# Kernel tuning notes

Hardware: AMD Instinct MI355X
Metric: run time of the kernel (lower is better)

The kernel has to match this reference:

```python
import jax, jax.numpy as jnp
import numpy as np
from jax import lax

B = 8192
HS = 64        # hidden_size (output channels)
HS4 = HS + 4   # internal channel count (68)
K = 3          # conv kernel size


def setup_inputs() -> dict:
    key = jax.random.key(0)
    ks = jax.random.split(key, 16)
    def n(k, shape, s=1.0):
        return jax.random.normal(k, shape, dtype=jnp.float32) * s
    return {
        "x": n(ks[0], (B, HS, 6, 6)),
        "cell": n(ks[1], (B, 2)),
        "interspace_coord": n(ks[2], (B, 2, 6, 6)),
        "conv1_w": n(ks[3], (HS4, HS4, K, K), 0.05),
        "conv1_b": n(ks[4], (HS4,), 0.05),
        "conv3_w": n(ks[5], (HS4, HS4, K, K), 0.05),
        "conv3_b": n(ks[6], (HS4,), 0.05),
        "lin5_w": n(ks[7], (9 * HS, HS4 * 25), 0.02),
        "lin5_b": n(ks[8], (9 * HS,), 0.02),
        "lin4_w": n(ks[9], (9 * HS, HS4 * 16), 0.02),
        "lin4_b": n(ks[10], (9 * HS,), 0.02),
        "lin3_w": n(ks[11], (9 * HS, HS4 * 9), 0.02),
        "lin3_b": n(ks[12], (9 * HS,), 0.02),
        "final_w": n(ks[13], (HS, 9 * HS), 0.02),
        "final_b": n(ks[14], (HS,), 0.02),
    }


def _conv(z, w, b):
    # torch Conv2d with padding=k//2, stride 1 == SAME conv, NCHW/OIHW
    y = lax.conv_general_dilated(z, w, (1, 1), 'SAME',
                                 dimension_numbers=('NCHW', 'OIHW', 'NCHW'))
    return y + b[None, :, None, None]


def _corners(z, ws):
    # four corner windows, stacked on a new leading axis (corner-major)
    H, W = z.shape[-2:]
    return jnp.stack([z[..., :ws, :ws],
                      z[..., :ws, W - ws:],
                      z[..., H - ws:, :ws],
                      z[..., H - ws:, W - ws:]], axis=0)


def reference(x, cell, interspace_coord,
              conv1_w, conv1_b, conv3_w, conv3_b,
              lin5_w, lin5_b, lin4_w, lin4_b, lin3_w, lin3_b,
              final_w, final_b):
    Bn = x.shape[0]
    new_cell = jnp.broadcast_to(cell.reshape(Bn, -1)[:, :, None, None],
                                (Bn, 2, 6, 6))
    lins = {5: (lin5_w, lin5_b), 4: (lin4_w, lin4_b), 3: (lin3_w, lin3_b)}
    for ws in (5, 4, 3):
        z = jnp.concatenate([x, new_cell, interspace_coord], axis=1)  # [B,68,6,6]
        z = _corners(z, ws).reshape(-1, HS4, ws, ws)                  # [4B,68,ws,ws]
        z = jnp.sin(z) + jnp.cos(z)
        z = jax.nn.relu(_conv(z, conv1_w, conv1_b))
        z = jnp.sin(z) + jnp.cos(z)
        z = jax.nn.relu(_conv(z, conv3_w, conv3_b)).reshape(4, Bn, -1)
        Wl, bl = lins[ws]
        z = jax.nn.relu(z @ Wl.T + bl).reshape(4, Bn, HS, 3, 3)
        m = jnp.concatenate([z[0], z[1]], axis=-1)   # [B,64,3,6]
        n = jnp.concatenate([z[2], z[3]], axis=-1)
        x = jnp.concatenate([m, n], axis=-2)          # [B,64,6,6]
    ew = 3
    c = _corners(x, ew)                               # [4,B,64,3,3]
    c = c.reshape(4 * Bn, -1) @ final_w.T + final_b   # [4B,64]
    c = c.reshape(Bn, HS, 2, 2)                       # same flat-order reshape as torch
    xc = x[:, :, ew - 1:ew + 1, ew - 1:ew + 1]        # center 2x2
    return (xc * c).reshape(Bn, HS, -1)
```

## Files before the change

kernel.cpp:

```cpp
#include <hip/hip_runtime.h>
#include <hip/hip_bf16.h>
#include <cstdint>
#include <cstddef>

#define BN 8192
#define MTOT 32768

using bf16 = __hip_bfloat16;
typedef float f32x4 __attribute__((ext_vector_type(4)));
typedef short short8 __attribute__((ext_vector_type(8)));

__device__ __forceinline__ bf16 f2b(float v) { return __float2bfloat16(v); }
__device__ __forceinline__ float b2f(bf16 v) { return __bfloat162float(v); }
__device__ __forceinline__ float sincos_sum(float x) {
    return 1.41421356237f * __sinf(x + 0.78539816340f);
}

template<int WS> struct WsCfg;
template<> struct WsCfg<5> { static constexpr int KD = 1728, NP = 1792, KTRUE = 1700; };
template<> struct WsCfg<4> { static constexpr int KD = 1088, NP = 1152, KTRUE = 1088; };
template<> struct WsCfg<3> { static constexpr int KD = 640,  NP = 640,  KTRUE = 612;  };

template<int WS, bool SRC_F32>
__global__ __launch_bounds__(256)
void zprep_block(const float* __restrict__ xF, const bf16* __restrict__ xB,
                 const float* __restrict__ cell, const float* __restrict__ isc,
                 bf16* __restrict__ Z, int m0g, int CM)
{
    constexpr int KD = WsCfg<WS>::KD;
    constexpr int KTRUE = 68 * WS * WS;
    const int b = blockIdx.x, tid = threadIdx.x;
    __shared__ float s[68][37];

    for (int i = tid; i < 64 * 36; i += 256) {
        int ic = i / 36, off = i % 36;
        size_t idx = ((size_t)b * 64 + ic) * 36 + off;
        float t = SRC_F32 ? xF[idx] : b2f(xB[idx]);
        s[ic][off] = sincos_sum(t);
    }
    if (tid < 2) {
        float t = sincos_sum(cell[b * 2 + tid]);
        #pragma unroll
        for (int off = 0; off < 36; off++) s[64 + tid][off] = t;
    }
    if (tid >= 64 && tid < 136) {
        int j = tid - 64;
        int ic = j / 36, off = j % 36;
        s[66 + ic][off] = sincos_sum(isc[((size_t)b * 2 + ic) * 36 + off]);
    }
    __syncthreads();

    for (int i = tid; i < 4 * KD; i += 256) {
        int q = i / KD, k = i % KD;
        int gm = q * BN + b;
        if (gm < m0g || gm >= m0g + CM) continue;
        float v = 0.f;
        if (k < KTRUE) {
            int pi = k / 68, ic = k % 68;
            int r = (q >> 1) * (6 - WS) + pi / WS;
            int c = (q & 1) * (6 - WS) + pi % WS;
            v = s[ic][r * 6 + c];
        }
        Z[(size_t)(gm - m0g) * KD + k] = f2b(v);
    }
}

template<int WS>
__global__ void build_wdense(const float* __restrict__ w1, const float* __restrict__ w3,
                             bf16* __restrict__ W1d, bf16* __restrict__ W3d)
{
    constexpr int KD = WsCfg<WS>::KD, NP = WsCfg<WS>::NP;
    constexpr int KTRUE = 68 * WS * WS;
    constexpr unsigned per = (unsigned)NP * (unsigned)KD;
    unsigned e = blockIdx.x * 256u + threadIdx.x;
    if (e >= 2u * per) return;
    const float* src = (e < per) ? w1 : w3;
    bf16* dst = (e < per) ? W1d : W3d;
    unsigned i = (e < per) ? e : (e - per);
    int n = (int)(i / (unsigned)KD), k = (int)(i % (unsigned)KD);
    float v = 0.f;
    if (n < KTRUE && k < KTRUE) {
        int po = n / 68, oc = n % 68, ro = po / WS, co = po % WS;
        int pi = k / 68, ic = k % 68, ri = pi / WS, ci = pi % WS;
        int kr = ri - ro + 1, kc = ci - co + 1;
        if (kr >= 0 && kr < 3 && kc >= 0 && kc < 3)
            v = src[((oc * 68 + ic) * 3 + kr) * 3 + kc];
    }
    dst[i] = f2b(v);
}

template<int WS>
__global__ void repack_lin(const float* __restrict__ wl, bf16* __restrict__ WlP)
{
    constexpr int KD = WsCfg<WS>::KD;
    constexpr int KTRUE = 68 * WS * WS;
    unsigned e = blockIdx.x * 256u + threadIdx.x;
    if (e >= 640u * (unsigned)KD) return;
    int n = (int)(e / (unsigned)KD), k = (int)(e % (unsigned)KD);
    float v = 0.f;
    if (n < 576 && k < KTRUE) {
        int pi = k / 68, ic = k % 68;
        v = wl[(size_t)n * KTRUE + ic * (WS * WS) + pi];
    }
    WlP[e] = f2b(v);
}

__global__ void repack_fin(const float* __restrict__ fw, bf16* __restrict__ WfP)
{
    unsigned e = blockIdx.x * 256u + threadIdx.x;
    if (e >= 128u * 576u) return;
    unsigned n = e / 576u, k = e % 576u;
    WfP[e] = (n < 64u) ? f2b(fw[n * 576u + k]) : f2b(0.f);
}

__global__ void build_bias(const float* __restrict__ b1, const float* __restrict__ b3,
                           const float* __restrict__ bl5, const float* __restrict__ bl4,
                           const float* __restrict__ bl3, const float* __restrict__ bfin,
                           float* __restrict__ bias)
{
    int e = blockIdx.x * 256 + threadIdx.x;
    if (e >= 9216) return;
    float v = 0.f;
    if (e < 1792)      { int n = e;        if (n < 1700) v = b1[n % 68]; }
    else if (e < 3584) { int n = e - 1792; if (n < 1700) v = b3[n % 68]; }
    else if (e < 4736) { int n = e - 3584; if (n < 1088) v = b1[n % 68]; }
    else if (e < 5888) { int n = e - 4736; if (n < 1088) v = b3[n % 68]; }
    else if (e < 6528) { int n = e - 5888; if (n < 612)  v = b1[n % 68]; }
    else if (e < 7168) { int n = e - 6528; if (n < 612)  v = b3[n % 68]; }
    else if (e < 7808) { int n = e - 7168; if (n < 576)  v = bl5[n]; }
    else if (e < 8448) { int n = e - 7808; if (n < 576)  v = bl4[n]; }
    else if (e < 9088) { int n = e - 8448; if (n < 576)  v = bl3[n]; }
    else               { int n = e - 9088; if (n < 64)   v = bfin[n]; }
    bias[e] = v;
}

__global__ void afin_prep(const bf16* __restrict__ xb, bf16* __restrict__ Afin,
                          int m_start, int CM)
{
    unsigned e = blockIdx.x * 256u + threadIdx.x;
    if (e >= (unsigned)CM * 576u) return;
    int lm = (int)(e / 576u), k = (int)(e % 576u);
    int m = m_start + lm;
    int q = m >> 13, b = m & (BN - 1);
    int ch = k / 9, p = k % 9, pr = p / 3, pc = p % 3;
    int r = (q >> 1) * 3 + pr, c = (q & 1) * 3 + pc;
    Afin[e] = xb[((size_t)b * 64 + ch) * 36 + r * 6 + c];
}

__device__ __forceinline__ void gload_lds16(const bf16* g, const bf16* lds_wave_base)
{
    unsigned off = (unsigned)(uintptr_t)lds_wave_base;
    off = __builtin_amdgcn_readfirstlane(off);
    __builtin_amdgcn_global_load_lds((const __attribute__((address_space(1))) unsigned int*)g,
                                     (__attribute__((address_space(3))) unsigned int*)off,
                                     16, 0, 0);
}

__device__ __forceinline__ int imin(int a, int b) { return a < b ? a : b; }
__device__ __forceinline__ int imax(int a, int b) { return a > b ? a : b; }

template<int EPI, int WS>
__global__ __launch_bounds__(256)
void gemm_bt(const bf16* __restrict__ A, const bf16* __restrict__ Bm, int KD,
             const float* __restrict__ bias,
             bf16* __restrict__ C, int ldc, int nlimit,
             int m0g, bf16* __restrict__ xbuf_out,
             const bf16* __restrict__ xbuf_xc, float* __restrict__ outp)
{
    __shared__ bf16 As[128 * 32];
    __shared__ bf16 Bs[128 * 32];
    const int tid = threadIdx.x;
    const int wave = tid >> 6, lane = tid & 63;
    const int l15 = lane & 15, lq = lane >> 4;
    const int wr = (wave >> 1) * 64, wc = (wave & 1) * 64;
    const int n0 = blockIdx.x * 128, m0 = blockIdx.y * 128;

    int klo = 0, khi = KD;
    if (WS > 0) {
        constexpr int ROWLEN = WS * 68;
        int po_lo = imin(n0 / 68, WS * WS - 1);
        int po_hi = imin((n0 + 127) / 68, WS * WS - 1);
        int r_lo = imax(po_lo / WS - 1, 0);
        int r_hi = imin(po_hi / WS + 1, WS - 1);
        klo = (r_lo * ROWLEN) & ~31;
        khi = imin(KD, ((r_hi + 1) * ROWLEN + 31) & ~31);
    }

    const bf16* Ab = A + (size_t)m0 * KD;
    const bf16* Bb = Bm + (size_t)n0 * KD;
    const int srow = tid >> 2, scol = (tid & 3) * 8;
    const bf16* aG0 = Ab + (size_t)srow * KD + scol;
    const bf16* aG1 = Ab + (size_t)(srow + 64) * KD + scol;
    const bf16* bG0 = Bb + (size_t)srow * KD + scol;
    const bf16* bG1 = Bb + (size_t)(srow + 64) * KD + scol;
    const bf16* lA0 = &As[wave * 512];
    const bf16* lA1 = &As[2048 + wave * 512];
    const bf16* lB0 = &Bs[wave * 512];
    const bf16* lB1 = &Bs[2048 + wave * 512];

    f32x4 acc[4][4];
    #pragma unroll
    for (int i = 0; i < 4; i++)
        #pragma unroll
        for (int j = 0; j < 4; j++) { f32x4 z = {0.f, 0.f, 0.f, 0.f}; acc[i][j] = z; }

    for (int k0 = klo; k0 < khi; k0 += 32) {
        gload_lds16(aG0 + k0, lA0);
        gload_lds16(aG1 + k0, lA1);
        gload_lds16(bG0 + k0, lB0);
        gload_lds16(bG1 + k0, lB1);
        __syncthreads();
        short8 af[4], bg[4];
        #pragma unroll
        for (int i = 0; i < 4; i++) af[i] = *(const short8*)&As[(wr + i * 16 + l15) * 32 + lq * 8];
        #pragma unroll
        for (int j = 0; j < 4; j++) bg[j] = *(const short8*)&Bs[(wc + j * 16 + l15) * 32 + lq * 8];
        #pragma unroll
        for (int i = 0; i < 4; i++)
            #pragma unroll
            for (int j = 0; j < 4; j++)
                acc[i][j] = __builtin_amdgcn_mfma_f32_16x16x32_bf16(af[i], bg[j], acc[i][j], 0, 0, 0);
        __syncthreads();
    }

    #pragma unroll
    for (int i = 0; i < 4; i++) {
        #pragma unroll
        for (int j = 0; j < 4; j++) {
            int n = n0 + wc + j * 16 + l15;
            #pragma unroll
            for (int r = 0; r < 4; r++) {
                int m = m0 + wr + i * 16 + lq * 4 + r;
                float v = acc[i][j][r];
                if (EPI == 0) {
                    if (n < nlimit) {
                        v += bias[n]; v = fmaxf(v, 0.f); v = sincos_sum(v);
                        C[(size_t)m * ldc + n] = f2b(v);
                    }
                } else if (EPI == 1) {
                    if (n < nlimit) {
                        v += bias[n]; v = fmaxf(v, 0.f);
                        C[(size_t)m * ldc + n] = f2b(v);
                    }
                } else if (EPI == 2) {
                    if (n < 576) {
                        v += bias[n]; v = fmaxf(v, 0.f);
                        int gm = m0g + m;
                        int q = gm >> 13, b = gm & (BN - 1);
                        int ch = n / 9, p = n % 9, rr = p / 3, cc = p % 3;
                        int R = rr + (q >> 1) * 3, Cc = cc + (q & 1) * 3;
                        xbuf_out[((size_t)b * 64 + ch) * 36 + R * 6 + Cc] = f2b(v);
                    }
                } else {
                    if (n < 64) {
                        v += bias[n];
                        int gm = m0g + m;
                        int f = gm * 64 + n;
                        int b2 = f >> 8, rem = f & 255;
                        int ch2 = rem >> 2, ii = (rem >> 1) & 1, jj = rem & 1;
                        float xc = b2f(xbuf_xc[((size_t)b2 * 64 + ch2) * 36 + (2 + ii) * 6 + (2 + jj)]);
                        outp[f] = v * xc;
                    }
                }
            }
        }
    }
}

template<int WS, bool SRC_F32>
static void run_ws(const float* xsrcF, const bf16* xsrcB, bf16* xdst,
                   const float* cell, const float* isc,
                   bf16* Za, bf16* Zb, const bf16* W1d, const bf16* W3d, const bf16* WlP,
                   const float* bias, int bo1, int bo3, int bol,
                   int nchunk, hipStream_t stream)
{
    constexpr int KD = WsCfg<WS>::KD, NP = WsCfg<WS>::NP;
    int CM = MTOT / nchunk;
    for (int c = 0; c < nchunk; c++) {
        int m0g = c * CM;
        zprep_block<WS, SRC_F32><<<BN, 256, 0, stream>>>(
            xsrcF, xsrcB, cell, isc, Za, m0g, CM);
        dim3 g12(NP / 128, CM / 128);
        gemm_bt<0, WS><<<g12, 256, 0, stream>>>(Za, W1d, KD, bias + bo1, Zb, KD, KD,
                                                0, nullptr, nullptr, nullptr);
        gemm_bt<1, WS><<<g12, 256, 0, stream>>>(Zb, W3d, KD, bias + bo3, Za, KD, KD,
                                                0, nullptr, nullptr, nullptr);
        dim3 g3(5, CM / 128);
        gemm_bt<2, 0><<<g3, 256, 0, stream>>>(Za, WlP, KD, bias + bol, nullptr, 0, 0,
                                              m0g, xdst, nullptr, nullptr);
    }
}

extern "C" void kernel_launch(void* const* d_in, const int* in_sizes, int n_in,
                              void* d_out, int out_size, void* d_ws, size_t ws_size,
                              hipStream_t stream)
{
    const float* x    = (const float*)d_in[0];
    const float* cell = (const float*)d_in[1];
    const float* isc  = (const float*)d_in[2];
    const float* c1w  = (const float*)d_in[3];
    const float* c1b  = (const float*)d_in[4];
    const float* c3w  = (const float*)d_in[5];
    const float* c3b  = (const float*)d_in[6];
    const float* l5w  = (const float*)d_in[7];
    const float* l5b  = (const float*)d_in[8];
    const float* l4w  = (const float*)d_in[9];
    const float* l4b  = (const float*)d_in[10];
    const float* l3w  = (const float*)d_in[11];
    const float* l3b  = (const float*)d_in[12];
    const float* fw   = (const float*)d_in[13];
    const float* fb   = (const float*)d_in[14];

    char* base = (char*)d_ws;
    size_t cur = 0;
    auto take = [&](size_t bytes) -> char* {
        char* r = base + cur; cur += (bytes + 255) & ~(size_t)255; return r;
    };

    const size_t XB = (size_t)BN * 64 * 36 * 2;
    size_t wbytes = 2 * (1792ull * 1728 + 1152ull * 1088 + 640ull * 640) * 2
                  + (640ull * 1728 + 640ull * 1088 + 640ull * 640) * 2
                  + 128ull * 576 * 2 + 9216ull * 4 + 64 * 256;
    auto need = [&](int nc) -> size_t {
        size_t xb = (nc > 1) ? 2 * XB : XB;
        return xb + wbytes + 2 * ((size_t)(MTOT / nc) * 1728 * 2);
    };
    int nchunk = (ws_size >= need(1)) ? 1 : (ws_size >= need(2)) ? 2
               : (ws_size >= need(4)) ? 4 : 8;

    bf16* xbufA = (bf16*)take(XB);
    bf16* xbufB = (nchunk > 1) ? (bf16*)take(XB) : xbufA;
    bf16* w1d5 = (bf16*)take(1792ull * 1728 * 2);
    bf16* w3d5 = (bf16*)take(1792ull * 1728 * 2);
    bf16* w1d4 = (bf16*)take(1152ull * 1088 * 2);
    bf16* w3d4 = (bf16*)take(1152ull * 1088 * 2);
    bf16* w1d3 = (bf16*)take(640ull * 640 * 2);
    bf16* w3d3 = (bf16*)take(640ull * 640 * 2);
    bf16* wl5p = (bf16*)take(640ull * 1728 * 2);
    bf16* wl4p = (bf16*)take(640ull * 1088 * 2);
    bf16* wl3p = (bf16*)take(640ull * 640 * 2);
    bf16* wfp  = (bf16*)take(128ull * 576 * 2);
    float* biasb = (float*)take(9216ull * 4);
    int CM = MTOT / nchunk;
    bf16* Za = (bf16*)take((size_t)CM * 1728 * 2);
    bf16* Zb = (bf16*)take((size_t)CM * 1728 * 2);
    bf16* Afin = Za;

    auto nb = [](size_t t) { return dim3((unsigned)((t + 255) / 256)); };
    build_wdense<5><<<nb(2ull * 1792 * 1728), 256, 0, stream>>>(c1w, c3w, w1d5, w3d5);
    build_wdense<4><<<nb(2ull * 1152 * 1088), 256, 0, stream>>>(c1w, c3w, w1d4, w3d4);
    build_wdense<3><<<nb(2ull * 640 * 640), 256, 0, stream>>>(c1w, c3w, w1d3, w3d3);
    repack_lin<5><<<nb(640ull * 1728), 256, 0, stream>>>(l5w, wl5p);
    repack_lin<4><<<nb(640ull * 1088), 256, 0, stream>>>(l4w, wl4p);
    repack_lin<3><<<nb(640ull * 640), 256, 0, stream>>>(l3w, wl3p);
    repack_fin<<<nb(128ull * 576), 256, 0, stream>>>(fw, wfp);
    build_bias<<<36, 256, 0, stream>>>(c1b, c3b, l5b, l4b, l3b, fb, biasb);

    run_ws<5, true >(x, nullptr, xbufA, cell, isc, Za, Zb, w1d5, w3d5, wl5p, biasb, 0,    1792, 7168, nchunk, stream);
    run_ws<4, false>(nullptr, xbufA, xbufB, cell, isc, Za, Zb, w1d4, w3d4, wl4p, biasb, 3584, 4736, 7808, nchunk, stream);
    run_ws<3, false>(nullptr, xbufB, xbufA, cell, isc, Za, Zb, w1d3, w3d3, wl3p, biasb, 5888, 6528, 8448, nchunk, stream);

    for (int c = 0; c < nchunk; c++) {
        int m0g = c * CM;
        afin_prep<<<nb((size_t)CM * 576), 256, 0, stream>>>(xbufA, Afin, m0g, CM);
        gemm_bt<3, 0><<<dim3(1, CM / 128), 256, 0, stream>>>(Afin, wfp, 576, biasb + 9088,
                                                             nullptr, 0, 0, m0g, nullptr,
                                                             xbufA, (float*)d_out);
    }
}
```

Baseline: 1.462 ms.

## Use XCD-aware atomic tile scheduling and a 64-wide K step in the GEMMs

```diff
diff --git a/kernel.cpp b/kernel.cpp
--- a/kernel.cpp
+++ b/kernel.cpp
@@ -159,21 +159,50 @@
 __device__ __forceinline__ int imin(int a, int b) { return a < b ? a : b; }
 __device__ __forceinline__ int imax(int a, int b) { return a > b ? a : b; }
 
+__device__ __forceinline__ int get_xcd()
+{
+    int x;
+    asm volatile("s_getreg_b32 %0, hwreg(HW_REG_XCC_ID)" : "=s"(x));
+    return x & 7;
+}
+
 template<int EPI, int WS>
 __global__ __launch_bounds__(256)
 void gemm_bt(const bf16* __restrict__ A, const bf16* __restrict__ Bm, int KD,
-             const float* __restrict__ bias,
+             const float* __restrict__ bias, int ntiles, int mt8, int quota,
+             unsigned* __restrict__ cnt,
              bf16* __restrict__ C, int ldc, int nlimit,
              int m0g, bf16* __restrict__ xbuf_out,
              const bf16* __restrict__ xbuf_xc, float* __restrict__ outp)
 {
-    __shared__ bf16 As[128 * 32];
-    __shared__ bf16 Bs[128 * 32];
+    __shared__ bf16 As[2 * 128 * 64];
+    __shared__ bf16 Bs[2 * 128 * 64];
+    __shared__ int s_tile;
     const int tid = threadIdx.x;
+
+    if (tid == 0) {
+        int xcd = get_xcd();
+        int t = -1;
+        for (int pass = 0; pass < 16 && t < 0; pass++) {
+            for (int k = 0; k < 8 && t < 0; k++) {
+                int q = (xcd + k) & 7;
+                unsigned idx = atomicAdd(&cnt[q], 1u);
+                if (idx < (unsigned)quota) t = q * quota + (int)idx;
+            }
+        }
+        if (t < 0) t = (int)blockIdx.x;
+        s_tile = t;
+    }
+    __syncthreads();
+    const int tile = s_tile;
+    const int qx = tile / quota, lt = tile % quota;
+    const int m_idx = qx * mt8 + lt / ntiles;
+    const int n_idx = lt % ntiles;
+    const int n0 = n_idx * 128, m0 = m_idx * 128;
+
     const int wave = tid >> 6, lane = tid & 63;
     const int l15 = lane & 15, lq = lane >> 4;
     const int wr = (wave >> 1) * 64, wc = (wave & 1) * 64;
-    const int n0 = blockIdx.x * 128, m0 = blockIdx.y * 128;
 
     int klo = 0, khi = KD;
     if (WS > 0) {
@@ -182,9 +211,13 @@
         int po_hi = imin((n0 + 127) / 68, WS * WS - 1);
         int r_lo = imax(po_lo / WS - 1, 0);
         int r_hi = imin(po_hi / WS + 1, WS - 1);
-        klo = (r_lo * ROWLEN) & ~31;
-        khi = imin(KD, ((r_hi + 1) * ROWLEN + 31) & ~31);
-    }
+        klo = (r_lo * ROWLEN) & ~63;
+        khi = imin(KD, ((r_hi + 1) * ROWLEN + 63) & ~63);
+    }
+
+    float bj[4];
+    #pragma unroll
+    for (int j = 0; j < 4; j++) bj[j] = bias[n0 + wc + j * 16 + l15];
 
     const bf16* Ab = A + (size_t)m0 * KD;
     const bf16* Bb = Bm + (size_t)n0 * KD;
@@ -193,10 +226,6 @@
     const bf16* aG1 = Ab + (size_t)(srow + 64) * KD + scol;
     const bf16* bG0 = Bb + (size_t)srow * KD + scol;
     const bf16* bG1 = Bb + (size_t)(srow + 64) * KD + scol;
-    const bf16* lA0 = &As[wave * 512];
-    const bf16* lA1 = &As[2048 + wave * 512];
-    const bf16* lB0 = &Bs[wave * 512];
-    const bf16* lB1 = &Bs[2048 + wave * 512];
 
     f32x4 acc[4][4];
     #pragma unroll
@@ -204,22 +233,30 @@
         #pragma unroll
         for (int j = 0; j < 4; j++) { f32x4 z = {0.f, 0.f, 0.f, 0.f}; acc[i][j] = z; }
 
-    for (int k0 = klo; k0 < khi; k0 += 32) {
-        gload_lds16(aG0 + k0, lA0);
-        gload_lds16(aG1 + k0, lA1);
-        gload_lds16(bG0 + k0, lB0);
-        gload_lds16(bG1 + k0, lB1);
+    for (int k0 = klo; k0 < khi; k0 += 64) {
+        #pragma unroll
+        for (int c = 0; c < 2; c++) {
+            gload_lds16(aG0 + k0 + c * 32, &As[c * 4096 + wave * 512]);
+            gload_lds16(aG1 + k0 + c * 32, &As[c * 4096 + 2048 + wave * 512]);
+            gload_lds16(bG0 + k0 + c * 32, &Bs[c * 4096 + wave * 512]);
+            gload_lds16(bG1 + k0 + c * 32, &Bs[c * 4096 + 2048 + wave * 512]);
+        }
         __syncthreads();
-        short8 af[4], bg[4];
         #pragma unroll
-        for (int i = 0; i < 4; i++) af[i] = *(const short8*)&As[(wr + i * 16 + l15) * 32 + lq * 8];
-        #pragma unroll
-        for (int j = 0; j < 4; j++) bg[j] = *(const short8*)&Bs[(wc + j * 16 + l15) * 32 + lq * 8];
-        #pragma unroll
-        for (int i = 0; i < 4; i++)
+        for (int c = 0; c < 2; c++) {
+            short8 af[4], bg[4];
+            #pragma unroll
+            for (int i = 0; i < 4; i++)
+                af[i] = *(const short8*)&As[c * 4096 + (wr + i * 16 + l15) * 32 + lq * 8];
             #pragma unroll
             for (int j = 0; j < 4; j++)
-                acc[i][j] = __builtin_amdgcn_mfma_f32_16x16x32_bf16(af[i], bg[j], acc[i][j], 0, 0, 0);
+                bg[j] = *(const short8*)&Bs[c * 4096 + (wc + j * 16 + l15) * 32 + lq * 8];
+            #pragma unroll
+            for (int i = 0; i < 4; i++)
+                #pragma unroll
+                for (int j = 0; j < 4; j++)
+                    acc[i][j] = __builtin_amdgcn_mfma_f32_16x16x32_bf16(af[i], bg[j], acc[i][j], 0, 0, 0);
+        }
         __syncthreads();
     }
 
@@ -234,17 +271,17 @@
                 float v = acc[i][j][r];
                 if (EPI == 0) {
                     if (n < nlimit) {
-                        v += bias[n]; v = fmaxf(v, 0.f); v = sincos_sum(v);
+                        v += bj[j]; v = fmaxf(v, 0.f); v = sincos_sum(v);
                         C[(size_t)m * ldc + n] = f2b(v);
                     }
                 } else if (EPI == 1) {
                     if (n < nlimit) {
-                        v += bias[n]; v = fmaxf(v, 0.f);
+                        v += bj[j]; v = fmaxf(v, 0.f);
                         C[(size_t)m * ldc + n] = f2b(v);
                     }
                 } else if (EPI == 2) {
                     if (n < 576) {
-                        v += bias[n]; v = fmaxf(v, 0.f);
+                        v += bj[j]; v = fmaxf(v, 0.f);
                         int gm = m0g + m;
                         int q = gm >> 13, b = gm & (BN - 1);
                         int ch = n / 9, p = n % 9, rr = p / 3, cc = p % 3;
@@ -253,7 +290,7 @@
                     }
                 } else {
                     if (n < 64) {
-                        v += bias[n];
+                        v += bj[j];
                         int gm = m0g + m;
                         int f = gm * 64 + n;
                         int b2 = f >> 8, rem = f & 255;
@@ -272,22 +309,22 @@
                    const float* cell, const float* isc,
                    bf16* Za, bf16* Zb, const bf16* W1d, const bf16* W3d, const bf16* WlP,
                    const float* bias, int bo1, int bo3, int bol,
-                   int nchunk, hipStream_t stream)
+                   int nchunk, unsigned* cnts, int* cset, hipStream_t stream)
 {
     constexpr int KD = WsCfg<WS>::KD, NP = WsCfg<WS>::NP;
     int CM = MTOT / nchunk;
+    int mt = CM / 128, mt8 = mt / 8;
     for (int c = 0; c < nchunk; c++) {
         int m0g = c * CM;
         zprep_block<WS, SRC_F32><<<BN, 256, 0, stream>>>(
             xsrcF, xsrcB, cell, isc, Za, m0g, CM);
-        dim3 g12(NP / 128, CM / 128);
-        gemm_bt<0, WS><<<g12, 256, 0, stream>>>(Za, W1d, KD, bias + bo1, Zb, KD, KD,
-                                                0, nullptr, nullptr, nullptr);
-        gemm_bt<1, WS><<<g12, 256, 0, stream>>>(Zb, W3d, KD, bias + bo3, Za, KD, KD,
-                                                0, nullptr, nullptr, nullptr);
-        dim3 g3(5, CM / 128);
-        gemm_bt<2, 0><<<g3, 256, 0, stream>>>(Za, WlP, KD, bias + bol, nullptr, 0, 0,
-                                              m0g, xdst, nullptr, nullptr);
+        int nt12 = NP / 128, q12 = nt12 * mt8;
+        gemm_bt<0, WS><<<nt12 * mt, 256, 0, stream>>>(Za, W1d, KD, bias + bo1,
+            nt12, mt8, q12, cnts + 8 * (*cset)++, Zb, KD, KD, 0, nullptr, nullptr, nullptr);
+        gemm_bt<1, WS><<<nt12 * mt, 256, 0, stream>>>(Zb, W3d, KD, bias + bo3,
+            nt12, mt8, q12, cnts + 8 * (*cset)++, Za, KD, KD, 0, nullptr, nullptr, nullptr);
+        gemm_bt<2, 0><<<5 * mt, 256, 0, stream>>>(Za, WlP, KD, bias + bol,
+            5, mt8, 5 * mt8, cnts + 8 * (*cset)++, nullptr, 0, 0, m0g, xdst, nullptr, nullptr);
     }
 }
 
@@ -320,7 +357,7 @@
     const size_t XB = (size_t)BN * 64 * 36 * 2;
     size_t wbytes = 2 * (1792ull * 1728 + 1152ull * 1088 + 640ull * 640) * 2
                   + (640ull * 1728 + 640ull * 1088 + 640ull * 640) * 2
-                  + 128ull * 576 * 2 + 9216ull * 4 + 64 * 256;
+                  + 128ull * 576 * 2 + 9216ull * 4 + 128ull * 8 * 4 + 64 * 256;
     auto need = [&](int nc) -> size_t {
         size_t xb = (nc > 1) ? 2 * XB : XB;
         return xb + wbytes + 2 * ((size_t)(MTOT / nc) * 1728 * 2);
@@ -341,10 +378,13 @@
     bf16* wl3p = (bf16*)take(640ull * 640 * 2);
     bf16* wfp  = (bf16*)take(128ull * 576 * 2);
     float* biasb = (float*)take(9216ull * 4);
+    unsigned* cnts = (unsigned*)take(128ull * 8 * 4);
     int CM = MTOT / nchunk;
     bf16* Za = (bf16*)take((size_t)CM * 1728 * 2);
     bf16* Zb = (bf16*)take((size_t)CM * 1728 * 2);
     bf16* Afin = Za;
+
+    hipMemsetAsync(cnts, 0, 128ull * 8 * 4, stream);
 
     auto nb = [](size_t t) { return dim3((unsigned)((t + 255) / 256)); };
     build_wdense<5><<<nb(2ull * 1792 * 1728), 256, 0, stream>>>(c1w, c3w, w1d5, w3d5);
@@ -356,15 +396,20 @@
     repack_fin<<<nb(128ull * 576), 256, 0, stream>>>(fw, wfp);
     build_bias<<<36, 256, 0, stream>>>(c1b, c3b, l5b, l4b, l3b, fb, biasb);
 
-    run_ws<5, true >(x, nullptr, xbufA, cell, isc, Za, Zb, w1d5, w3d5, wl5p, biasb, 0,    1792, 7168, nchunk, stream);
-    run_ws<4, false>(nullptr, xbufA, xbufB, cell, isc, Za, Zb, w1d4, w3d4, wl4p, biasb, 3584, 4736, 7808, nchunk, stream);
-    run_ws<3, false>(nullptr, xbufB, xbufA, cell, isc, Za, Zb, w1d3, w3d3, wl3p, biasb, 5888, 6528, 8448, nchunk, stream);
+    int cset = 0;
+    run_ws<5, true >(x, nullptr, xbufA, cell, isc, Za, Zb, w1d5, w3d5, wl5p, biasb,
+                     0, 1792, 7168, nchunk, cnts, &cset, stream);
+    run_ws<4, false>(nullptr, xbufA, xbufB, cell, isc, Za, Zb, w1d4, w3d4, wl4p, biasb,
+                     3584, 4736, 7808, nchunk, cnts, &cset, stream);
+    run_ws<3, false>(nullptr, xbufB, xbufA, cell, isc, Za, Zb, w1d3, w3d3, wl3p, biasb,
+                     5888, 6528, 8448, nchunk, cnts, &cset, stream);
 
     for (int c = 0; c < nchunk; c++) {
         int m0g = c * CM;
+        int mt = CM / 128, mt8 = mt / 8;
         afin_prep<<<nb((size_t)CM * 576), 256, 0, stream>>>(xbufA, Afin, m0g, CM);
-        gemm_bt<3, 0><<<dim3(1, CM / 128), 256, 0, stream>>>(Afin, wfp, 576, biasb + 9088,
-                                                             nullptr, 0, 0, m0g, nullptr,
-                                                             xbufA, (float*)d_out);
-    }
-}
+        gemm_bt<3, 0><<<mt, 256, 0, stream>>>(Afin, wfp, 576, biasb + 9088,
+            1, mt8, mt8, cnts + 8 * cset++, nullptr, 0, 0, m0g, nullptr,
+            xbufA, (float*)d_out);
+    }
+}
```

Measured after the change: 1.391 ms. 1.05x faster.
